# Kernel optimization log

Measured on AMD Instinct MI355X. Metric: run time of the kernel, lower is better.

The kernel has to match this reference:

```python
import jax, jax.numpy as jnp
import numpy as np

M_CONST = 0.05  # monotonicity margin m from __init__ default


def setup_inputs() -> dict:
    key = jax.random.key(0)
    ks = jax.random.split(key, 5)
    B, IN, OUT = 262144, 128, 128
    scale = 1.0 / np.sqrt(IN)
    return {
        "x": jax.random.normal(ks[0], (B, IN), dtype=jnp.float32),
        "z": jax.random.normal(ks[1], (B, OUT), dtype=jnp.float32),
        "U_w": jax.random.normal(ks[2], (OUT, IN), dtype=jnp.float32) * scale,
        "U_b": jax.random.normal(ks[3], (OUT,), dtype=jnp.float32) * scale,
        "A_w": jax.random.normal(ks[4], (OUT, OUT), dtype=jnp.float32) * scale,
        "d": jnp.zeros((OUT,), dtype=jnp.float32),
    }


def reference(x, z, U_w, U_b, A_w, d):
    # U(x) = x @ U_w.T + U_b
    ux = x @ U_w.T + U_b
    # rowSums diag: diag(|A| @ 1) -> per-output-row abs row sums; z @ diag(r) = z * r
    row_sums = jnp.sum(jnp.abs(A_w), axis=1)  # [OUT]
    dw = jnp.exp(d)                            # diag weights
    # transformedA = diag(1/dw) @ A @ diag(dw); z @ transformedA.T = ((z*dw) @ A.T) * (1/dw)
    z_lin = ((z * dw) @ A_w.T) / dw
    z_out = M_CONST * z + z_lin - z * row_sums
    return (ux + z_out,)
```

## Files before the change

### kernel.cpp

```cpp
#include <hip/hip_runtime.h>
#include <hip/hip_bf16.h>

typedef __attribute__((ext_vector_type(8)))  float f8;
typedef __attribute__((ext_vector_type(16))) float f32x16;
typedef __attribute__((ext_vector_type(8)))  short bf8;

__device__ __forceinline__ short f2bf(float f) {
    unsigned u = __builtin_bit_cast(unsigned, f);
    u += 0x7fff + ((u >> 16) & 1);
    return (short)(u >> 16);
}

__global__ void nemon_prep(const float* __restrict__ Uw,
                           const float* __restrict__ Aw,
                           const float* __restrict__ dvec,
                           short* __restrict__ pre)
{
    __shared__ float rs[128], dwv[128];
    const int tid = threadIdx.x;
    if (tid < 128) {
        float s = 0.f;
        #pragma unroll 8
        for (int k = 0; k < 128; ++k) s += fabsf(Aw[tid * 128 + k]);
        rs[tid]  = s;
        dwv[tid] = expf(dvec[tid]);
    }
    __syncthreads();
    #pragma unroll
    for (int half = 0; half < 2; ++half) {
        const int e    = blockIdx.x * 512 + half * 256 + tid;
        const int j    = e & 7;
        const int lane = (e >> 3) & 63;
        const int f    = e >> 9;
        const int nt   = f & 3;
        const int kt   = f >> 2;
        const int k    = kt * 16 + (lane >> 5) * 8 + j;
        const int n    = nt * 32 + (lane & 31);
        float v;
        if (k < 128) {
            v = Uw[n * 128 + k];
        } else {
            const int k2 = k - 128;
            v = Aw[n * 128 + k2] * (dwv[k2] / dwv[n]);
            if (n == k2) v += 0.05f - rs[n];
        }
        pre[e] = f2bf(v);
    }
}

__global__ __launch_bounds__(256, 1) void nemon_main(
    const float* __restrict__ x,
    const float* __restrict__ z,
    const float* __restrict__ Ub,
    const short* __restrict__ pre,
    float* __restrict__ out)
{
    __shared__ short W[32768];
    const int tid = threadIdx.x;

    {
        const int4* src = (const int4*)pre;
        int4*       dst = (int4*)W;
        #pragma unroll
        for (int i = 0; i < 16; ++i) dst[tid + 256 * i] = src[tid + 256 * i];
    }
    __syncthreads();

    const int wave = tid >> 6;
    const int lane = tid & 63;
    const int lo   = lane & 31;
    const int hi   = lane >> 5;

    const int  wgid = blockIdx.x * 4 + wave;
    const long TROW = (long)2048 * 32;

    float ubv[4];
    #pragma unroll
    for (int nt = 0; nt < 4; ++nt) ubv[nt] = Ub[nt * 32 + lo];

    const long   R0 = (long)wgid * 32;
    const float* xr = x + (R0 + lo) * 128 + hi * 8;
    const float* zr = z + (R0 + lo) * 128 + hi * 8;

    f8 bufA[8], bufB[8];
    #pragma unroll
    for (int i = 0; i < 8; ++i) bufA[i] = *(const f8*)(xr + i * 16);
    #pragma unroll
    for (int i = 0; i < 8; ++i) bufB[i] = *(const f8*)(zr + i * 16);

    #pragma unroll
    for (int it = 0; it < 4; ++it) {
        f32x16 acc[4];
        #pragma unroll
        for (int nt = 0; nt < 4; ++nt) {
            #pragma unroll
            for (int r = 0; r < 16; ++r) acc[nt][r] = ubv[nt];
        }

        #pragma unroll
        for (int kt = 0; kt < 8; ++kt) {
            bf8 a = { f2bf(bufA[kt][0]), f2bf(bufA[kt][1]), f2bf(bufA[kt][2]), f2bf(bufA[kt][3]),
                      f2bf(bufA[kt][4]), f2bf(bufA[kt][5]), f2bf(bufA[kt][6]), f2bf(bufA[kt][7]) };
            #pragma unroll
            for (int nt = 0; nt < 4; ++nt) {
                bf8 b = *(const bf8*)&W[((kt * 4 + nt) * 64 + lane) * 8];
                acc[nt] = __builtin_amdgcn_mfma_f32_32x32x16_bf16(a, b, acc[nt], 0, 0, 0);
            }
        }
        if (it < 3) {
            const float* nx = xr + (long)(it + 1) * TROW * 128;
            #pragma unroll
            for (int i = 0; i < 8; ++i) bufA[i] = *(const f8*)(nx + i * 16);
        }

        #pragma unroll
        for (int kt = 0; kt < 8; ++kt) {
            bf8 a = { f2bf(bufB[kt][0]), f2bf(bufB[kt][1]), f2bf(bufB[kt][2]), f2bf(bufB[kt][3]),
                      f2bf(bufB[kt][4]), f2bf(bufB[kt][5]), f2bf(bufB[kt][6]), f2bf(bufB[kt][7]) };
            #pragma unroll
            for (int nt = 0; nt < 4; ++nt) {
                bf8 b = *(const bf8*)&W[(((kt + 8) * 4 + nt) * 64 + lane) * 8];
                acc[nt] = __builtin_amdgcn_mfma_f32_32x32x16_bf16(a, b, acc[nt], 0, 0, 0);
            }
        }
        if (it < 3) {
            const float* nz = zr + (long)(it + 1) * TROW * 128;
            #pragma unroll
            for (int i = 0; i < 8; ++i) bufB[i] = *(const f8*)(nz + i * 16);
        }

        float* ob = out + (R0 + (long)it * TROW) * 128;
        #pragma unroll
        for (int reg = 0; reg < 16; ++reg) {
            const int rowA = (reg & 3) + 8 * (reg >> 2) + 4 * hi;
            #pragma unroll
            for (int nt = 0; nt < 4; ++nt)
                ob[rowA * 128 + nt * 32 + lo] = acc[nt][reg];
        }
    }
}

extern "C" void kernel_launch(void* const* d_in, const int* in_sizes, int n_in,
                              void* d_out, int out_size, void* d_ws, size_t ws_size,
                              hipStream_t stream) {
    const float* x  = (const float*)d_in[0];
    const float* z  = (const float*)d_in[1];
    const float* Uw = (const float*)d_in[2];
    const float* Ub = (const float*)d_in[3];
    const float* Aw = (const float*)d_in[4];
    const float* dv = (const float*)d_in[5];
    float* out = (float*)d_out;
    short* pre = (short*)d_ws;

    nemon_prep<<<64, 256, 0, stream>>>(Uw, Aw, dv, pre);
    nemon_main<<<512, 256, 0, stream>>>(x, z, Ub, pre, out);
}
```

Measured before the change: 107.6 us.

## Double main-kernel grid with fewer row tiles per wave; use packed bf16 convert

Launches 1024 blocks instead of 512, so each wave handles 2 row tiles instead of 4, with the tile stride adjusted to match. The scalar round-to-nearest float-to-bf16 bit manipulation is replaced by the hardware v_cvt_pk_bf16_f32 instruction, which converts two values per instruction. More blocks should spread the memory-bound work across more CUs and cut per-wave conversion ALU work. In exchange the 64KB weight copy into LDS is repeated by twice as many blocks, and the launch bound of one block per CU limits overlap.

```diff
diff --git a/kernel.cpp b/kernel.cpp
--- a/kernel.cpp
+++ b/kernel.cpp
@@ -9,6 +9,12 @@
     unsigned u = __builtin_bit_cast(unsigned, f);
     u += 0x7fff + ((u >> 16) & 1);
     return (short)(u >> 16);
+}
+
+__device__ __forceinline__ unsigned cvt_pk_bf16(float a, float b) {
+    unsigned r;
+    asm("v_cvt_pk_bf16_f32 %0, %1, %2" : "=v"(r) : "v"(a), "v"(b));
+    return r;
 }
 
 __global__ void nemon_prep(const float* __restrict__ Uw,
@@ -72,7 +78,7 @@
     const int hi   = lane >> 5;
 
     const int  wgid = blockIdx.x * 4 + wave;
-    const long TROW = (long)2048 * 32;
+    const long TROW = (long)4096 * 32;
 
     float ubv[4];
     #pragma unroll
@@ -89,7 +95,7 @@
     for (int i = 0; i < 8; ++i) bufB[i] = *(const f8*)(zr + i * 16);
 
     #pragma unroll
-    for (int it = 0; it < 4; ++it) {
+    for (int it = 0; it < 2; ++it) {
         f32x16 acc[4];
         #pragma unroll
         for (int nt = 0; nt < 4; ++nt) {
@@ -99,32 +105,38 @@
 
         #pragma unroll
         for (int kt = 0; kt < 8; ++kt) {
-            bf8 a = { f2bf(bufA[kt][0]), f2bf(bufA[kt][1]), f2bf(bufA[kt][2]), f2bf(bufA[kt][3]),
-                      f2bf(bufA[kt][4]), f2bf(bufA[kt][5]), f2bf(bufA[kt][6]), f2bf(bufA[kt][7]) };
+            union { bf8 b; unsigned u[4]; } a;
+            a.u[0] = cvt_pk_bf16(bufA[kt][0], bufA[kt][1]);
+            a.u[1] = cvt_pk_bf16(bufA[kt][2], bufA[kt][3]);
+            a.u[2] = cvt_pk_bf16(bufA[kt][4], bufA[kt][5]);
+            a.u[3] = cvt_pk_bf16(bufA[kt][6], bufA[kt][7]);
             #pragma unroll
             for (int nt = 0; nt < 4; ++nt) {
                 bf8 b = *(const bf8*)&W[((kt * 4 + nt) * 64 + lane) * 8];
-                acc[nt] = __builtin_amdgcn_mfma_f32_32x32x16_bf16(a, b, acc[nt], 0, 0, 0);
+                acc[nt] = __builtin_amdgcn_mfma_f32_32x32x16_bf16(a.b, b, acc[nt], 0, 0, 0);
             }
         }
-        if (it < 3) {
-            const float* nx = xr + (long)(it + 1) * TROW * 128;
+        if (it == 0) {
+            const float* nx = xr + TROW * 128;
             #pragma unroll
             for (int i = 0; i < 8; ++i) bufA[i] = *(const f8*)(nx + i * 16);
         }
 
         #pragma unroll
         for (int kt = 0; kt < 8; ++kt) {
-            bf8 a = { f2bf(bufB[kt][0]), f2bf(bufB[kt][1]), f2bf(bufB[kt][2]), f2bf(bufB[kt][3]),
-                      f2bf(bufB[kt][4]), f2bf(bufB[kt][5]), f2bf(bufB[kt][6]), f2bf(bufB[kt][7]) };
+            union { bf8 b; unsigned u[4]; } a;
+            a.u[0] = cvt_pk_bf16(bufB[kt][0], bufB[kt][1]);
+            a.u[1] = cvt_pk_bf16(bufB[kt][2], bufB[kt][3]);
+            a.u[2] = cvt_pk_bf16(bufB[kt][4], bufB[kt][5]);
+            a.u[3] = cvt_pk_bf16(bufB[kt][6], bufB[kt][7]);
             #pragma unroll
             for (int nt = 0; nt < 4; ++nt) {
                 bf8 b = *(const bf8*)&W[(((kt + 8) * 4 + nt) * 64 + lane) * 8];
-                acc[nt] = __builtin_amdgcn_mfma_f32_32x32x16_bf16(a, b, acc[nt], 0, 0, 0);
+                acc[nt] = __builtin_amdgcn_mfma_f32_32x32x16_bf16(a.b, b, acc[nt], 0, 0, 0);
             }
         }
-        if (it < 3) {
-            const float* nz = zr + (long)(it + 1) * TROW * 128;
+        if (it == 0) {
+            const float* nz = zr + TROW * 128;
             #pragma unroll
             for (int i = 0; i < 8; ++i) bufB[i] = *(const f8*)(nz + i * 16);
         }
@@ -153,5 +165,5 @@
     short* pre = (short*)d_ws;
 
     nemon_prep<<<64, 256, 0, stream>>>(Uw, Aw, dv, pre);
-    nemon_main<<<512, 256, 0, stream>>>(x, z, Ub, pre, out);
+    nemon_main<<<1024, 256, 0, stream>>>(x, z, Ub, pre, out);
 }
```

Result: faster. 96.98 us (-9.8%).
